# Performance work log

Hardware: AMD Instinct MI355X
Metric: run time of the kernel (lower is better)

The kernel has to match this reference:

```python
import jax, jax.numpy as jnp
import numpy as np

N_SIDE = 64
P = N_SIDE * N_SIDE          # n_patch = 4096
B = 8                        # n_batch
H = 32                       # n_hidden
E = H + 2                    # mhsa embed_dim = 34
N_OBS = 10
N_PRED = 50


def _neighbor_flat():
    # Reproduce the module's boundary-corrected 3x3 neighborhood indices.
    idx = np.arange(P)
    rows, cols = idx // N_SIDE, idx % N_SIDE
    off = np.array([[-1, -1], [-1, 0], [-1, 1], [0, -1], [0, 0], [0, 1], [1, -1], [1, 0], [1, 1]])
    nr = (rows[:, None] + off[:, 0]).reshape(N_SIDE, N_SIDE, 9)
    nc = (cols[:, None] + off[:, 1]).reshape(N_SIDE, N_SIDE, 9)
    nr[0] += 1; nr[-1] -= 1          # shift edge rows inward
    nc[:, 0] += 1; nc[:, -1] -= 1    # shift edge cols inward
    return jnp.asarray((nr * N_SIDE + nc).reshape(P, 9))

NEIGH = _neighbor_flat()  # (P, 9) flat patch indices


def _patch_label():
    r = (np.arange(N_SIDE) / N_SIDE).astype(np.float32)
    lab = np.stack(np.meshgrid(r, r, indexing='ij'), axis=-1).reshape(P, 2)
    return jnp.asarray(lab)

LABEL = _patch_label()  # (P, 2) normalized (row, col) coords


def _layernorm(x, g, b, eps=1e-5):
    m = x.mean(-1, keepdims=True)
    v = ((x - m) ** 2).mean(-1, keepdims=True)
    return (x - m) * jax.lax.rsqrt(v + eps) * g + b


def _step(h, params):
    # One local-attention step: h (B*P, H) -> layernorm(fc2(h + fc_sa(attn_center)))
    ipw, ipb, opw, opb, saw, sab, f2w, f2b, lg, lb = params
    q = h.reshape(B, P, H).transpose(1, 0, 2)                       # (P, B, H)
    lab = jnp.broadcast_to(LABEL[:, None, :], (P, B, 2))
    q = jnp.concatenate([q, lab], axis=-1)                          # (P, B, E)
    tok = q[NEIGH]                                                  # (P, 9, B, E) neighbor gather
    tok = tok.transpose(1, 2, 0, 3).reshape(9, B * P, E)            # (S=9, N, E)
    qkv = tok @ ipw.T + ipb                                         # (9, N, 3E)
    qq, kk, vv = jnp.split(qkv, 3, axis=-1)
    scores = jnp.einsum('sne,tne->nst', qq, kk) / jnp.sqrt(jnp.float32(E))
    w = jax.nn.softmax(scores, axis=-1)                             # (N, 9, 9)
    av = jnp.einsum('nst,tne->sne', w, vv)                          # (9, N, E)
    av = av @ opw.T + opb
    new_h = h + av[4] @ saw.T + sab                                 # center token + residual
    return _layernorm(new_h @ f2w.T + f2b, lg, lb)


def setup_inputs() -> dict:
    key = jax.random.key(0)
    ks = jax.random.split(key, 10)
    s = 0.05
    return {
        'x': jax.random.normal(ks[0], (N_OBS, B * P, H), jnp.float32),
        'in_proj_w': jax.random.normal(ks[1], (3 * E, E), jnp.float32) * s,
        'in_proj_b': jax.random.normal(ks[2], (3 * E,), jnp.float32) * s,
        'out_proj_w': jax.random.normal(ks[3], (E, E), jnp.float32) * s,
        'out_proj_b': jax.random.normal(ks[4], (E,), jnp.float32) * s,
        'fc_sa_w': jax.random.normal(ks[5], (H, E), jnp.float32) * s,
        'fc_sa_b': jax.random.normal(ks[6], (H,), jnp.float32) * s,
        'fc2_w': jax.random.normal(ks[7], (H, H), jnp.float32) * s,
        'fc2_b': jax.random.normal(ks[8], (H,), jnp.float32) * s,
        'ln2_g': jnp.ones((H,), jnp.float32),
        'ln2_b': jnp.zeros((H,), jnp.float32),
    }


def reference(x, in_proj_w, in_proj_b, out_proj_w, out_proj_b, fc_sa_w, fc_sa_b, fc2_w, fc2_b, ln2_g, ln2_b):
    params = (in_proj_w, in_proj_b, out_proj_w, out_proj_b, fc_sa_w, fc_sa_b, fc2_w, fc2_b, ln2_g, ln2_b)
    # Observation phase: 10 independent steps over x[t] -> vmap over time.
    obs = jax.vmap(lambda xt: _step(xt, params))(x)                 # (N_OBS, N, H)
    # Prediction phase: 50 sequential steps rolling on the last prediction.
    def scan_fn(h, _):
        p = _step(h, params)
        return p, p
    _, preds = jax.lax.scan(scan_fn, obs[-1], None, length=N_PRED)  # (N_PRED, N, H)
    return jnp.concatenate([obs, preds], axis=0)                    # (60, B*P, H)
```

## Files before the change

kernel.cpp:

```cpp
#include <hip/hip_runtime.h>
#include <hip/hip_bf16.h>

typedef __hip_bfloat16 bf16;
typedef unsigned short u16;
typedef unsigned int   u32;

#define PP    4096
#define HH    32
#define NTOK  32768
#define NSTEP 60
#define NOBS  10
#define SKK   35
#define SVP   33

#define OFF_WIN  0
#define OFF_BIN  3672
#define OFF_WFSA 3776
#define OFF_BFSA 4928
#define OFF_F2W  4960
#define OFF_F2B  5984
#define OFF_LNG  6016
#define OFF_LNB  6048
#define OFF_WVP  6080
#define OFF_BVP  7232
#define WGT_FLOATS 7264
#define WGT_BYTES  (7296 * 4)

__device__ __forceinline__ float bb(bf16 v) { return __bfloat162float(v); }

__device__ __forceinline__ int detect_f32(const u16* raw) {
  int bad = 0;
#pragma unroll
  for (int i = 0; i < 40; i++) {
    float f = __uint_as_float(((u32)raw[2 * i]) << 16);
    bad |= !(fabsf(f) < 1.0f);
  }
  return bad;
}

__device__ __forceinline__ float rdw(const void* p, int i, int f32) {
  return f32 ? ((const float*)p)[i] : bb(((const bf16*)p)[i]);
}

__device__ __forceinline__ void load_h(const void* hsrc, int hf32, int n, float* he) {
  if (hf32) {
    const float4* p = (const float4*)((const float*)hsrc + (size_t)n * HH);
#pragma unroll
    for (int k = 0; k < 8; k++) {
      float4 v = p[k];
      he[4 * k] = v.x; he[4 * k + 1] = v.y; he[4 * k + 2] = v.z; he[4 * k + 3] = v.w;
    }
  } else {
    const uint4* p = (const uint4*)((const bf16*)hsrc + (size_t)n * HH);
#pragma unroll
    for (int k = 0; k < 4; k++) {
      uint4 v = p[k];
      u32 w[4] = {v.x, v.y, v.z, v.w};
#pragma unroll
      for (int m = 0; m < 4; m++) {
        he[8 * k + 2 * m]     = __uint_as_float(w[m] << 16);
        he[8 * k + 2 * m + 1] = __uint_as_float(w[m] & 0xffff0000u);
      }
    }
  }
}

__device__ __forceinline__ void load_h8(const void* hsrc, int hf32, int n, int off, float* o8) {
  if (hf32) {
    const float4* p = (const float4*)((const float*)hsrc + (size_t)n * HH + off);
    float4 a = p[0], b = p[1];
    o8[0]=a.x; o8[1]=a.y; o8[2]=a.z; o8[3]=a.w;
    o8[4]=b.x; o8[5]=b.y; o8[6]=b.z; o8[7]=b.w;
  } else {
    uint4 v = *(const uint4*)((const bf16*)hsrc + (size_t)n * HH + off);
    u32 w[4] = {v.x, v.y, v.z, v.w};
#pragma unroll
    for (int m = 0; m < 4; m++) {
      o8[2 * m]     = __uint_as_float(w[m] << 16);
      o8[2 * m + 1] = __uint_as_float(w[m] & 0xffff0000u);
    }
  }
}

__global__ void prep_kernel(const void* __restrict__ ipw, const void* __restrict__ ipb,
                            const void* __restrict__ opw, const void* __restrict__ opb,
                            const void* __restrict__ saw, const void* __restrict__ sab,
                            const void* __restrict__ f2w, const void* __restrict__ f2b,
                            const void* __restrict__ lng, const void* __restrict__ lnb,
                            float* __restrict__ gw) {
  const int f32 = detect_f32((const u16*)ipw);
  int i = blockIdx.x * blockDim.x + threadIdx.x;
  if (i < 3672) { int r = i / 36, e = i - r * 36;
    gw[OFF_WIN + i] = (e < 34) ? rdw(ipw, r * 34 + e, f32) : 0.f; return; }
  i -= 3672;
  if (i < 104)  { gw[OFF_BIN + i] = (i < 102) ? rdw(ipb, i, f32) : 0.f; return; }
  i -= 104;
  if (i < 1152) { int r = i / 36, e = i - r * 36; float a = 0.f;
    if (e < 34) for (int f = 0; f < 34; f++)
      a += rdw(saw, r * 34 + f, f32) * rdw(opw, f * 34 + e, f32);
    gw[OFF_WFSA + i] = a; return; }
  i -= 1152;
  if (i < 32)   { float a = rdw(sab, i, f32);
    for (int f = 0; f < 34; f++) a += rdw(saw, i * 34 + f, f32) * rdw(opb, f, f32);
    gw[OFF_BFSA + i] = a; return; }
  i -= 32;
  if (i < 1024) { gw[OFF_F2W + i] = rdw(f2w, i, f32); return; }
  i -= 1024;
  if (i < 32)   { gw[OFF_F2B + i] = rdw(f2b, i, f32); return; }
  i -= 32;
  if (i < 32)   { gw[OFF_LNG + i] = rdw(lng, i, f32); return; }
  i -= 32;
  if (i < 32)   { gw[OFF_LNB + i] = rdw(lnb, i, f32); return; }
  i -= 32;
  if (i < 1152) {
    int r = i / 36, e = i - r * 36; float a = 0.f;
    if (e < 34) {
      for (int f = 0; f < 34; f++) {
        float wf = 0.f;
        for (int g = 0; g < 34; g++)
          wf += rdw(saw, r * 34 + g, f32) * rdw(opw, g * 34 + f, f32);
        a += wf * rdw(ipw, (68 + f) * 34 + e, f32);
      }
    }
    gw[OFF_WVP + i] = a; return; }
  i -= 1152;
  if (i < 32) {
    float a = rdw(sab, i, f32);
    for (int g = 0; g < 34; g++) a += rdw(saw, i * 34 + g, f32) * rdw(opb, g, f32);
    for (int f = 0; f < 34; f++) {
      float wf = 0.f;
      for (int g = 0; g < 34; g++)
        wf += rdw(saw, i * 34 + g, f32) * rdw(opw, g * 34 + f, f32);
      a += wf * rdw(ipb, 68 + f, f32);
    }
    gw[OFF_BVP + i] = a; return; }
}

__global__ __launch_bounds__(512, 4)
void step_kernel(int t0, const void* __restrict__ x, void* __restrict__ out,
                 const float* __restrict__ gw,
                 const void* __restrict__ ipw, const void* __restrict__ ipb,
                 const void* __restrict__ opw, const void* __restrict__ opb,
                 const void* __restrict__ saw, const void* __restrict__ sab,
                 const void* __restrict__ f2w, const void* __restrict__ f2b,
                 const void* __restrict__ lng, const void* __restrict__ lnb,
                 float* __restrict__ hb0) {
  __shared__ float s_k [256 * SKK];
  __shared__ float s_vp[256 * SVP];
  __shared__ float s_wvp[32 * 36 + 32];

  const int f32 = detect_f32((const u16*)ipw);
  const int tt = threadIdx.x;
  const int tstep = t0 + blockIdx.y;
  const int b  = blockIdx.x >> 5;
  const int r0 = (blockIdx.x & 31) << 1;

  const void* hsrc; int hf32;
  if (tstep < NOBS) {
    hsrc = f32 ? (const void*)((const float*)x + (size_t)tstep * NTOK * HH)
               : (const void*)((const bf16*)x + (size_t)tstep * NTOK * HH);
    hf32 = f32;
  } else if (f32) {
    hsrc = (const void*)((const float*)out + (size_t)(tstep - 1) * NTOK * HH); hf32 = 1;
  } else if (hb0) {
    hsrc = (const void*)(hb0 + (size_t)((tstep - 1) & 1) * NTOK * HH); hf32 = 1;
  } else {
    hsrc = (const void*)((const bf16*)out + (size_t)(tstep - 1) * NTOK * HH); hf32 = 0;
  }

  if (!gw) {
    for (int i = tt; i < 32 * 36 + 32; i += 512) {
      if (i < 32 * 36) {
        int r = i / 36, e = i - r * 36; float a = 0.f;
        if (e < 34) {
          for (int f = 0; f < 34; f++) {
            float wf = 0.f;
            for (int g = 0; g < 34; g++)
              wf += rdw(saw, r * 34 + g, f32) * rdw(opw, g * 34 + f, f32);
            a += wf * rdw(ipw, (68 + f) * 34 + e, f32);
          }
        }
        s_wvp[i] = a;
      } else {
        int r = i - 32 * 36;
        float a = rdw(sab, r, f32);
        for (int g = 0; g < 34; g++) a += rdw(saw, r * 34 + g, f32) * rdw(opb, g, f32);
        for (int f = 0; f < 34; f++) {
          float wf = 0.f;
          for (int g = 0; g < 34; g++)
            wf += rdw(saw, r * 34 + g, f32) * rdw(opw, g * 34 + f, f32);
          a += wf * rdw(ipb, 68 + f, f32);
        }
        s_wvp[i] = a;
      }
    }
    __syncthreads();
  }

  {
    const int a_idx = tt & 255;
    const int a_half = tt >> 8;
    const int tr = a_idx >> 6, col = a_idx & 63;
    int grow = r0 - 1 + tr; grow = max(0, min(63, grow));
    float he[36];
    load_h(hsrc, hf32, b * PP + grow * 64 + col, he);
    he[32] = grow * (1.f / 64.f); he[33] = col * (1.f / 64.f);
    he[34] = 0.f; he[35] = 0.f;

    if (a_half == 0) {
      float* dst = s_k + a_idx * SKK;
      if (gw) {
#pragma unroll
        for (int j = 0; j < 34; j++) {
          const float4* w4 = (const float4*)(gw + OFF_WIN + (34 + j) * 36);
          float acc = gw[OFF_BIN + 34 + j];
#pragma unroll
          for (int g = 0; g < 9; g++) {
            float4 w = w4[g];
            acc += w.x * he[4*g] + w.y * he[4*g+1] + w.z * he[4*g+2] + w.w * he[4*g+3];
          }
          dst[j] = acc;
        }
      } else {
        for (int j = 0; j < 34; j++) {
          float acc = rdw(ipb, 34 + j, f32);
          for (int e = 0; e < 34; e++) acc += rdw(ipw, (34 + j) * 34 + e, f32) * he[e];
          dst[j] = acc;
        }
      }
    } else {
      float* dst = s_vp + a_idx * SVP;
      if (gw) {
#pragma unroll
        for (int j = 0; j < 32; j++) {
          const float4* w4 = (const float4*)(gw + OFF_WVP + j * 36);
          float acc = gw[OFF_BVP + j];
#pragma unroll
          for (int g = 0; g < 9; g++) {
            float4 w = w4[g];
            acc += w.x * he[4*g] + w.y * he[4*g+1] + w.z * he[4*g+2] + w.w * he[4*g+3];
          }
          dst[j] = acc;
        }
      } else {
        for (int j = 0; j < 32; j++) {
          float acc = s_wvp[32 * 36 + j];
          const float* wr = s_wvp + j * 36;
          for (int e = 0; e < 34; e++) acc += wr[e] * he[e];
          dst[j] = acc;
        }
      }
    }
  }
  __syncthreads();

  const int tl = tt >> 2, qd = tt & 3;
  const int prow = r0 + (tl >> 6), pcol = tl & 63;
  const int rr = prow + (prow == 0) - (prow == 63);
  const int cc = pcol + (pcol == 0) - (pcol == 63);
  const int np = b * PP + prow * 64 + pcol;

  const int e0 = (qd < 2) ? qd * 9 : 18 + (qd - 2) * 8;
  const int ne = (qd < 2) ? 9 : 8;

  float hq[36];
  load_h(hsrc, hf32, b * PP + rr * 64 + cc, hq);
  hq[32] = rr * (1.f / 64.f); hq[33] = cc * (1.f / 64.f);
  hq[34] = 0.f; hq[35] = 0.f;

  float q[9];
#pragma unroll
  for (int jj = 0; jj < 9; jj++) {
    float a = 0.f;
    if (jj < ne) {
      const int row = e0 + jj;
      if (gw) {
        const float4* w4 = (const float4*)(gw + OFF_WIN + row * 36);
        a = gw[OFF_BIN + row];
#pragma unroll
        for (int g = 0; g < 9; g++) {
          float4 w = w4[g];
          a += w.x * hq[4*g] + w.y * hq[4*g+1] + w.z * hq[4*g+2] + w.w * hq[4*g+3];
        }
      } else {
        a = rdw(ipb, row, f32);
        for (int e = 0; e < 34; e++) a += rdw(ipw, row * 34 + e, f32) * hq[e];
      }
    }
    q[jj] = a;
  }

  int lts[9];
#pragma unroll
  for (int dr = 0; dr < 3; dr++)
#pragma unroll
    for (int dc = 0; dc < 3; dc++)
      lts[dr * 3 + dc] = (rr - r0 + dr) * 64 + (cc - 1 + dc);

  float w9[9];
  float mx = -1e30f;
#pragma unroll
  for (int tn = 0; tn < 9; tn++) {
    const float* kp = s_k + lts[tn] * SKK + e0;
    float a = 0.f;
#pragma unroll
    for (int jj = 0; jj < 9; jj++)
      if (jj < ne) a += q[jj] * kp[jj];
    a += __shfl_xor(a, 1);
    a += __shfl_xor(a, 2);
    w9[tn] = a * 0.17149858514250882f;
    mx = fmaxf(mx, w9[tn]);
  }
  float ssum = 0.f;
#pragma unroll
  for (int tn = 0; tn < 9; tn++) { w9[tn] = expf(w9[tn] - mx); ssum += w9[tn]; }
  const float inv = 1.f / ssum;
#pragma unroll
  for (int tn = 0; tn < 9; tn++) w9[tn] *= inv;

  float he8[8];
  load_h8(hsrc, hf32, np, qd * 8, he8);

  float nh8[8];
#pragma unroll
  for (int k = 0; k < 8; k++) nh8[k] = he8[k];
#pragma unroll
  for (int tn = 0; tn < 9; tn++) {
    const float wv = w9[tn];
    const float* vp = s_vp + lts[tn] * SVP + qd * 8;
#pragma unroll
    for (int k = 0; k < 8; k++) nh8[k] += wv * vp[k];
  }

  float y[32];
#pragma unroll
  for (int j = 0; j < 32; j++) {
    float a;
    if (gw) {
      const float4* w4 = (const float4*)(gw + OFF_F2W + j * 32 + qd * 8);
      float4 wa = w4[0], wb = w4[1];
      a = wa.x * nh8[0] + wa.y * nh8[1] + wa.z * nh8[2] + wa.w * nh8[3]
        + wb.x * nh8[4] + wb.y * nh8[5] + wb.z * nh8[6] + wb.w * nh8[7];
    } else {
      a = 0.f;
      for (int k2 = 0; k2 < 8; k2++) a += rdw(f2w, j * 32 + qd * 8 + k2, f32) * nh8[k2];
    }
    a += __shfl_xor(a, 1);
    a += __shfl_xor(a, 2);
    y[j] = a + (gw ? gw[OFF_F2B + j] : rdw(f2b, j, f32));
  }

  float m = 0.f;
#pragma unroll
  for (int j = 0; j < 32; j++) m += y[j];
  m *= (1.f / 32.f);
  float var = 0.f;
#pragma unroll
  for (int j = 0; j < 32; j++) { float d = y[j] - m; var += d * d; }
  var *= (1.f / 32.f);
  float rstd = rsqrtf(var + 1e-5f);
  rstd = rstd * (1.5f - 0.5f * (var + 1e-5f) * rstd * rstd);

  float o8[8];
#pragma unroll
  for (int k = 0; k < 8; k++) {
    float v01 = (qd & 1) ? y[8 + k]  : y[k];
    float v23 = (qd & 1) ? y[24 + k] : y[16 + k];
    float vy  = (qd & 2) ? v23 : v01;
    float g  = gw ? gw[OFF_LNG + qd * 8 + k] : rdw(lng, qd * 8 + k, f32);
    float b2 = gw ? gw[OFF_LNB + qd * 8 + k] : rdw(lnb, qd * 8 + k, f32);
    o8[k] = (vy - m) * rstd * g + b2;
  }

  const size_t obase = ((size_t)tstep * NTOK + np) * HH + qd * 8;
  if (f32) {
    float4* po = (float4*)((float*)out + obase);
    po[0] = make_float4(o8[0], o8[1], o8[2], o8[3]);
    po[1] = make_float4(o8[4], o8[5], o8[6], o8[7]);
  } else {
    u32 pk[4];
#pragma unroll
    for (int k2 = 0; k2 < 4; k2++) {
      bf16 b0 = __float2bfloat16(o8[2 * k2]);
      bf16 b1 = __float2bfloat16(o8[2 * k2 + 1]);
      pk[k2] = (u32)*reinterpret_cast<u16*>(&b0)
             | ((u32)*reinterpret_cast<u16*>(&b1) << 16);
    }
    *(uint4*)((bf16*)out + obase) = make_uint4(pk[0], pk[1], pk[2], pk[3]);
    if (hb0 && tstep >= NOBS - 1) {
      float4* ph = (float4*)(hb0 + (size_t)(tstep & 1) * NTOK * HH + (size_t)np * HH + qd * 8);
      ph[0] = make_float4(o8[0], o8[1], o8[2], o8[3]);
      ph[1] = make_float4(o8[4], o8[5], o8[6], o8[7]);
    }
  }
}

extern "C" void kernel_launch(void* const* d_in, const int* in_sizes, int n_in,
                              void* d_out, int out_size, void* d_ws, size_t ws_size,
                              hipStream_t stream) {
  const void* x = d_in[0];
  float* gw  = (ws_size >= (size_t)WGT_BYTES) ? (float*)d_ws : nullptr;
  float* hb0 = (ws_size >= (size_t)WGT_BYTES + 2ull * NTOK * HH * 4)
                 ? (float*)((char*)d_ws + WGT_BYTES) : nullptr;

  if (gw)
    prep_kernel<<<29, 256, 0, stream>>>(d_in[1], d_in[2], d_in[3], d_in[4], d_in[5],
                                        d_in[6], d_in[7], d_in[8], d_in[9], d_in[10], gw);

  step_kernel<<<dim3(256, NOBS), 512, 0, stream>>>(0, x, d_out, gw,
                                       d_in[1], d_in[2], d_in[3], d_in[4], d_in[5],
                                       d_in[6], d_in[7], d_in[8], d_in[9], d_in[10],
                                       hb0);

  for (int t = NOBS; t < NSTEP; t++) {
    step_kernel<<<dim3(256, 1), 512, 0, stream>>>(t, x, d_out, gw,
                                       d_in[1], d_in[2], d_in[3], d_in[4], d_in[5],
                                       d_in[6], d_in[7], d_in[8], d_in[9], d_in[10],
                                       hb0);
  }
}
```

Baseline: 2.507 ms.

## Double threads per block, splitting K/V projection and attention across more lanes

```diff
diff --git a/kernel.cpp b/kernel.cpp
--- a/kernel.cpp
+++ b/kernel.cpp
@@ -23,7 +23,6 @@
 #define OFF_LNB  6048
 #define OFF_WVP  6080
 #define OFF_BVP  7232
-#define WGT_FLOATS 7264
 #define WGT_BYTES  (7296 * 4)
 
 __device__ __forceinline__ float bb(bf16 v) { return __bfloat162float(v); }
@@ -42,6 +41,9 @@
   return f32 ? ((const float*)p)[i] : bb(((const bf16*)p)[i]);
 }
 
+__device__ __forceinline__ float upk_lo(u32 w) { return __uint_as_float(w << 16); }
+__device__ __forceinline__ float upk_hi(u32 w) { return __uint_as_float(w & 0xffff0000u); }
+
 __device__ __forceinline__ void load_h(const void* hsrc, int hf32, int n, float* he) {
   if (hf32) {
     const float4* p = (const float4*)((const float*)hsrc + (size_t)n * HH);
@@ -58,27 +60,63 @@
       u32 w[4] = {v.x, v.y, v.z, v.w};
 #pragma unroll
       for (int m = 0; m < 4; m++) {
-        he[8 * k + 2 * m]     = __uint_as_float(w[m] << 16);
-        he[8 * k + 2 * m + 1] = __uint_as_float(w[m] & 0xffff0000u);
-      }
-    }
-  }
-}
-
-__device__ __forceinline__ void load_h8(const void* hsrc, int hf32, int n, int off, float* o8) {
+        he[8 * k + 2 * m]     = upk_lo(w[m]);
+        he[8 * k + 2 * m + 1] = upk_hi(w[m]);
+      }
+    }
+  }
+}
+
+__device__ __forceinline__ void load_h_half(const void* hsrc, int hf32, int n, int half,
+                                            float fr, float fc, float* hp) {
+  if (half == 0) {
+    if (hf32) {
+      const float4* p = (const float4*)((const float*)hsrc + (size_t)n * HH);
+#pragma unroll
+      for (int k = 0; k < 5; k++) {
+        float4 v = p[k];
+        hp[4*k] = v.x; hp[4*k+1] = v.y; hp[4*k+2] = v.z; hp[4*k+3] = v.w;
+      }
+    } else {
+      const uint2* p = (const uint2*)((const bf16*)hsrc + (size_t)n * HH);
+#pragma unroll
+      for (int k = 0; k < 5; k++) {
+        uint2 v = p[k];
+        hp[4*k]   = upk_lo(v.x); hp[4*k+1] = upk_hi(v.x);
+        hp[4*k+2] = upk_lo(v.y); hp[4*k+3] = upk_hi(v.y);
+      }
+    }
+  } else {
+    if (hf32) {
+      const float4* p = (const float4*)((const float*)hsrc + (size_t)n * HH + 20);
+#pragma unroll
+      for (int k = 0; k < 3; k++) {
+        float4 v = p[k];
+        hp[4*k] = v.x; hp[4*k+1] = v.y; hp[4*k+2] = v.z; hp[4*k+3] = v.w;
+      }
+    } else {
+      const uint2* p = (const uint2*)((const bf16*)hsrc + (size_t)n * HH + 20);
+#pragma unroll
+      for (int k = 0; k < 3; k++) {
+        uint2 v = p[k];
+        hp[4*k]   = upk_lo(v.x); hp[4*k+1] = upk_hi(v.x);
+        hp[4*k+2] = upk_lo(v.y); hp[4*k+3] = upk_hi(v.y);
+      }
+    }
+    hp[12] = fr; hp[13] = fc;
+#pragma unroll
+    for (int k = 14; k < 20; k++) hp[k] = 0.f;
+  }
+}
+
+__device__ __forceinline__ void load_h4(const void* hsrc, int hf32, int n, int off, float* o4) {
   if (hf32) {
-    const float4* p = (const float4*)((const float*)hsrc + (size_t)n * HH + off);
-    float4 a = p[0], b = p[1];
-    o8[0]=a.x; o8[1]=a.y; o8[2]=a.z; o8[3]=a.w;
-    o8[4]=b.x; o8[5]=b.y; o8[6]=b.z; o8[7]=b.w;
-  } else {
-    uint4 v = *(const uint4*)((const bf16*)hsrc + (size_t)n * HH + off);
-    u32 w[4] = {v.x, v.y, v.z, v.w};
-#pragma unroll
-    for (int m = 0; m < 4; m++) {
-      o8[2 * m]     = __uint_as_float(w[m] << 16);
-      o8[2 * m + 1] = __uint_as_float(w[m] & 0xffff0000u);
-    }
+    float4 v = *(const float4*)((const float*)hsrc + (size_t)n * HH + off);
+    o4[0] = v.x; o4[1] = v.y; o4[2] = v.z; o4[3] = v.w;
+  } else {
+    uint2 v = *(const uint2*)((const bf16*)hsrc + (size_t)n * HH + off);
+    o4[0] = upk_lo(v.x); o4[1] = upk_hi(v.x);
+    o4[2] = upk_lo(v.y); o4[3] = upk_hi(v.y);
   }
 }
 
@@ -136,7 +174,7 @@
     gw[OFF_BVP + i] = a; return; }
 }
 
-__global__ __launch_bounds__(512, 4)
+__global__ __launch_bounds__(1024, 4)
 void step_kernel(int t0, const void* __restrict__ x, void* __restrict__ out,
                  const float* __restrict__ gw,
                  const void* __restrict__ ipw, const void* __restrict__ ipb,
@@ -169,7 +207,7 @@
   }
 
   if (!gw) {
-    for (int i = tt; i < 32 * 36 + 32; i += 512) {
+    for (int i = tt; i < 32 * 36 + 32; i += 1024) {
       if (i < 32 * 36) {
         int r = i / 36, e = i - r * 36; float a = 0.f;
         if (e < 34) {
@@ -198,51 +236,63 @@
   }
 
   {
-    const int a_idx = tt & 255;
-    const int a_half = tt >> 8;
+    const int a_task = tt >> 1;
+    const int half   = tt & 1;
+    const int a_idx  = a_task & 255;
+    const int a_kv   = a_task >> 8;
     const int tr = a_idx >> 6, col = a_idx & 63;
     int grow = r0 - 1 + tr; grow = max(0, min(63, grow));
-    float he[36];
-    load_h(hsrc, hf32, b * PP + grow * 64 + col, he);
-    he[32] = grow * (1.f / 64.f); he[33] = col * (1.f / 64.f);
-    he[34] = 0.f; he[35] = 0.f;
-
-    if (a_half == 0) {
-      float* dst = s_k + a_idx * SKK;
-      if (gw) {
+
+    float hp[20];
+    load_h_half(hsrc, hf32, b * PP + grow * 64 + col, half,
+                grow * (1.f / 64.f), col * (1.f / 64.f), hp);
+
+    if (gw) {
+      if (a_kv == 0) {
+        float* dst = s_k + a_idx * SKK;
 #pragma unroll
         for (int j = 0; j < 34; j++) {
-          const float4* w4 = (const float4*)(gw + OFF_WIN + (34 + j) * 36);
-          float acc = gw[OFF_BIN + 34 + j];
-#pragma unroll
-          for (int g = 0; g < 9; g++) {
+          const float4* w4 = (const float4*)(gw + OFF_WIN + (34 + j) * 36 + half * 20);
+          float acc = half ? 0.f : gw[OFF_BIN + 34 + j];
+#pragma unroll
+          for (int g = 0; g < 5; g++) {
             float4 w = w4[g];
-            acc += w.x * he[4*g] + w.y * he[4*g+1] + w.z * he[4*g+2] + w.w * he[4*g+3];
+            acc += w.x * hp[4*g] + w.y * hp[4*g+1] + w.z * hp[4*g+2] + w.w * hp[4*g+3];
           }
-          dst[j] = acc;
-        }
+          acc += __shfl_xor(acc, 1);
+          if (half == 0) dst[j] = acc;
+        }
+        if (half == 0) dst[34] = 0.f;
       } else {
+        float* dst = s_vp + a_idx * SVP;
+#pragma unroll
+        for (int j = 0; j < 32; j++) {
+          const float4* w4 = (const float4*)(gw + OFF_WVP + j * 36 + half * 20);
+          float acc = half ? 0.f : gw[OFF_BVP + j];
+#pragma unroll
+          for (int g = 0; g < 5; g++) {
+            float4 w = w4[g];
+            acc += w.x * hp[4*g] + w.y * hp[4*g+1] + w.z * hp[4*g+2] + w.w * hp[4*g+3];
+          }
+          acc += __shfl_xor(acc, 1);
+          if (half == 0) dst[j] = acc;
+        }
+      }
+    } else if (half == 0) {
+      float he[36];
+      load_h(hsrc, hf32, b * PP + grow * 64 + col, he);
+      he[32] = grow * (1.f / 64.f); he[33] = col * (1.f / 64.f);
+      he[34] = 0.f; he[35] = 0.f;
+      if (a_kv == 0) {
+        float* dst = s_k + a_idx * SKK;
         for (int j = 0; j < 34; j++) {
           float acc = rdw(ipb, 34 + j, f32);
           for (int e = 0; e < 34; e++) acc += rdw(ipw, (34 + j) * 34 + e, f32) * he[e];
           dst[j] = acc;
         }
-      }
-    } else {
-      float* dst = s_vp + a_idx * SVP;
-      if (gw) {
-#pragma unroll
-        for (int j = 0; j < 32; j++) {
-          const float4* w4 = (const float4*)(gw + OFF_WVP + j * 36);
-          float acc = gw[OFF_BVP + j];
-#pragma unroll
-          for (int g = 0; g < 9; g++) {
-            float4 w = w4[g];
-            acc += w.x * he[4*g] + w.y * he[4*g+1] + w.z * he[4*g+2] + w.w * he[4*g+3];
-          }
-          dst[j] = acc;
-        }
+        dst[34] = 0.f;
       } else {
+        float* dst = s_vp + a_idx * SVP;
         for (int j = 0; j < 32; j++) {
           float acc = s_wvp[32 * 36 + j];
           const float* wr = s_wvp + j * 36;
@@ -252,43 +302,48 @@
       }
     }
   }
-  __syncthreads();
-
-  const int tl = tt >> 2, qd = tt & 3;
+
+  const int tl = tt >> 3, od = tt & 7;
   const int prow = r0 + (tl >> 6), pcol = tl & 63;
   const int rr = prow + (prow == 0) - (prow == 63);
   const int cc = pcol + (pcol == 0) - (pcol == 63);
   const int np = b * PP + prow * 64 + pcol;
 
-  const int e0 = (qd < 2) ? qd * 9 : 18 + (qd - 2) * 8;
-  const int ne = (qd < 2) ? 9 : 8;
-
   float hq[36];
   load_h(hsrc, hf32, b * PP + rr * 64 + cc, hq);
   hq[32] = rr * (1.f / 64.f); hq[33] = cc * (1.f / 64.f);
   hq[34] = 0.f; hq[35] = 0.f;
 
-  float q[9];
-#pragma unroll
-  for (int jj = 0; jj < 9; jj++) {
-    float a = 0.f;
-    if (jj < ne) {
+  const int e0 = (od < 2) ? od * 5 : 10 + (od - 2) * 4;
+  float q[5];
+  if (gw) {
+#pragma unroll
+    for (int jj = 0; jj < 5; jj++) {
       const int row = e0 + jj;
-      if (gw) {
-        const float4* w4 = (const float4*)(gw + OFF_WIN + row * 36);
-        a = gw[OFF_BIN + row];
-#pragma unroll
-        for (int g = 0; g < 9; g++) {
-          float4 w = w4[g];
-          a += w.x * hq[4*g] + w.y * hq[4*g+1] + w.z * hq[4*g+2] + w.w * hq[4*g+3];
-        }
-      } else {
-        a = rdw(ipb, row, f32);
-        for (int e = 0; e < 34; e++) a += rdw(ipw, row * 34 + e, f32) * hq[e];
-      }
-    }
-    q[jj] = a;
-  }
+      const float4* w4 = (const float4*)(gw + OFF_WIN + row * 36);
+      float a = gw[OFF_BIN + row];
+#pragma unroll
+      for (int g = 0; g < 9; g++) {
+        float4 w = w4[g];
+        a += w.x * hq[4*g] + w.y * hq[4*g+1] + w.z * hq[4*g+2] + w.w * hq[4*g+3];
+      }
+      q[jj] = a;
+    }
+  } else {
+#pragma unroll
+    for (int jj = 0; jj < 5; jj++) {
+      const int row = e0 + jj;
+      float a = rdw(ipb, row, f32);
+      for (int e = 0; e < 34; e++) a += rdw(ipw, row * 34 + e, f32) * hq[e];
+      q[jj] = a;
+    }
+  }
+  if (od >= 2) q[4] = 0.f;
+
+  float he4[4];
+  load_h4(hsrc, hf32, np, od * 4, he4);
+
+  __syncthreads();
 
   int lts[9];
 #pragma unroll
@@ -304,10 +359,10 @@
     const float* kp = s_k + lts[tn] * SKK + e0;
     float a = 0.f;
 #pragma unroll
-    for (int jj = 0; jj < 9; jj++)
-      if (jj < ne) a += q[jj] * kp[jj];
+    for (int jj = 0; jj < 5; jj++) a += q[jj] * kp[jj];
     a += __shfl_xor(a, 1);
     a += __shfl_xor(a, 2);
+    a += __shfl_xor(a, 4);
     w9[tn] = a * 0.17149858514250882f;
     mx = fmaxf(mx, w9[tn]);
   }
@@ -318,18 +373,13 @@
 #pragma unroll
   for (int tn = 0; tn < 9; tn++) w9[tn] *= inv;
 
-  float he8[8];
-  load_h8(hsrc, hf32, np, qd * 8, he8);
-
-  float nh8[8];
-#pragma unroll
-  for (int k = 0; k < 8; k++) nh8[k] = he8[k];
+  float nh4[4] = {he4[0], he4[1], he4[2], he4[3]};
 #pragma unroll
   for (int tn = 0; tn < 9; tn++) {
     const float wv = w9[tn];
-    const float* vp = s_vp + lts[tn] * SVP + qd * 8;
-#pragma unroll
-    for (int k = 0; k < 8; k++) nh8[k] += wv * vp[k];
+    const float* vp = s_vp + lts[tn] * SVP + od * 4;
+#pragma unroll
+    for (int k = 0; k < 4; k++) nh4[k] += wv * vp[k];
   }
 
   float y[32];
@@ -337,16 +387,15 @@
   for (int j = 0; j < 32; j++) {
     float a;
     if (gw) {
-      const float4* w4 = (const float4*)(gw + OFF_F2W + j * 32 + qd * 8);
-      float4 wa = w4[0], wb = w4[1];
-      a = wa.x * nh8[0] + wa.y * nh8[1] + wa.z * nh8[2] + wa.w * nh8[3]
-        + wb.x * nh8[4] + wb.y * nh8[5] + wb.z * nh8[6] + wb.w * nh8[7];
+      float4 w = *(const float4*)(gw + OFF_F2W + j * 32 + od * 4);
+      a = w.x * nh4[0] + w.y * nh4[1] + w.z * nh4[2] + w.w * nh4[3];
     } else {
       a = 0.f;
-      for (int k2 = 0; k2 < 8; k2++) a += rdw(f2w, j * 32 + qd * 8 + k2, f32) * nh8[k2];
+      for (int k2 = 0; k2 < 4; k2++) a += rdw(f2w, j * 32 + od * 4 + k2, f32) * nh4[k2];
     }
     a += __shfl_xor(a, 1);
     a += __shfl_xor(a, 2);
+    a += __shfl_xor(a, 4);
     y[j] = a + (gw ? gw[OFF_F2B + j] : rdw(f2b, j, f32));
   }
 
@@ -361,36 +410,33 @@
   float rstd = rsqrtf(var + 1e-5f);
   rstd = rstd * (1.5f - 0.5f * (var + 1e-5f) * rstd * rstd);
 
-  float o8[8];
-#pragma unroll
-  for (int k = 0; k < 8; k++) {
-    float v01 = (qd & 1) ? y[8 + k]  : y[k];
-    float v23 = (qd & 1) ? y[24 + k] : y[16 + k];
-    float vy  = (qd & 2) ? v23 : v01;
-    float g  = gw ? gw[OFF_LNG + qd * 8 + k] : rdw(lng, qd * 8 + k, f32);
-    float b2 = gw ? gw[OFF_LNB + qd * 8 + k] : rdw(lnb, qd * 8 + k, f32);
-    o8[k] = (vy - m) * rstd * g + b2;
-  }
-
-  const size_t obase = ((size_t)tstep * NTOK + np) * HH + qd * 8;
+  float o4[4];
+#pragma unroll
+  for (int k = 0; k < 4; k++) {
+    float a0 = (od & 1) ? y[4 + k]  : y[k];
+    float a1 = (od & 1) ? y[12 + k] : y[8 + k];
+    float a2 = (od & 1) ? y[20 + k] : y[16 + k];
+    float a3 = (od & 1) ? y[28 + k] : y[24 + k];
+    float b0 = (od & 2) ? a1 : a0;
+    float b1 = (od & 2) ? a3 : a2;
+    float vy = (od & 4) ? b1 : b0;
+    float g  = gw ? gw[OFF_LNG + od * 4 + k] : rdw(lng, od * 4 + k, f32);
+    float b2 = gw ? gw[OFF_LNB + od * 4 + k] : rdw(lnb, od * 4 + k, f32);
+    o4[k] = (vy - m) * rstd * g + b2;
+  }
+
+  const size_t obase = ((size_t)tstep * NTOK + np) * HH + od * 4;
   if (f32) {
-    float4* po = (float4*)((float*)out + obase);
-    po[0] = make_float4(o8[0], o8[1], o8[2], o8[3]);
-    po[1] = make_float4(o8[4], o8[5], o8[6], o8[7]);
-  } else {
-    u32 pk[4];
-#pragma unroll
-    for (int k2 = 0; k2 < 4; k2++) {
-      bf16 b0 = __float2bfloat16(o8[2 * k2]);
-      bf16 b1 = __float2bfloat16(o8[2 * k2 + 1]);
-      pk[k2] = (u32)*reinterpret_cast<u16*>(&b0)
-             | ((u32)*reinterpret_cast<u16*>(&b1) << 16);
-    }
-    *(uint4*)((bf16*)out + obase) = make_uint4(pk[0], pk[1], pk[2], pk[3]);
+    *(float4*)((float*)out + obase) = make_float4(o4[0], o4[1], o4[2], o4[3]);
+  } else {
+    bf16 b0 = __float2bfloat16(o4[0]), b1 = __float2bfloat16(o4[1]);
+    bf16 b2 = __float2bfloat16(o4[2]), b3 = __float2bfloat16(o4[3]);
+    u32 p0 = (u32)*reinterpret_cast<u16*>(&b0) | ((u32)*reinterpret_cast<u16*>(&b1) << 16);
+    u32 p1 = (u32)*reinterpret_cast<u16*>(&b2) | ((u32)*reinterpret_cast<u16*>(&b3) << 16);
+    *(uint2*)((bf16*)out + obase) = make_uint2(p0, p1);
     if (hb0 && tstep >= NOBS - 1) {
-      float4* ph = (float4*)(hb0 + (size_t)(tstep & 1) * NTOK * HH + (size_t)np * HH + qd * 8);
-      ph[0] = make_float4(o8[0], o8[1], o8[2], o8[3]);
-      ph[1] = make_float4(o8[4], o8[5], o8[6], o8[7]);
+      *(float4*)(hb0 + (size_t)(tstep & 1) * NTOK * HH + (size_t)np * HH + od * 4)
+          = make_float4(o4[0], o4[1], o4[2], o4[3]);
     }
   }
 }
@@ -407,13 +453,13 @@
     prep_kernel<<<29, 256, 0, stream>>>(d_in[1], d_in[2], d_in[3], d_in[4], d_in[5],
                                         d_in[6], d_in[7], d_in[8], d_in[9], d_in[10], gw);
 
-  step_kernel<<<dim3(256, NOBS), 512, 0, stream>>>(0, x, d_out, gw,
+  step_kernel<<<dim3(256, NOBS), 1024, 0, stream>>>(0, x, d_out, gw,
                                        d_in[1], d_in[2], d_in[3], d_in[4], d_in[5],
                                        d_in[6], d_in[7], d_in[8], d_in[9], d_in[10],
                                        hb0);
 
   for (int t = NOBS; t < NSTEP; t++) {
-    step_kernel<<<dim3(256, 1), 512, 0, stream>>>(t, x, d_out, gw,
+    step_kernel<<<dim3(256, 1), 1024, 0, stream>>>(t, x, d_out, gw,
                                        d_in[1], d_in[2], d_in[3], d_in[4], d_in[5],
                                        d_in[6], d_in[7], d_in[8], d_in[9], d_in[10],
                                        hb0);
```

After: 4.174 ms. +66.5%, slower.
